# Kernel tuning notes

Measured on AMD Instinct MI355X. Metric: run time of the kernel, lower is better.

## Reference

```python
import jax, jax.numpy as jnp
import numpy as np

B, S, D = 8, 2048, 256
C, H = 32, 4
HD = D // H  # head_dim = 64


def setup_inputs() -> dict:
    key = jax.random.key(0)
    ks = jax.random.split(key, 12)
    scale = 0.02
    x = jax.random.normal(ks[0], (B, S, D), dtype=jnp.float32)
    conditioning = jax.random.uniform(ks[1], (B, S, C), dtype=jnp.float32)
    Wq_w = jax.random.normal(ks[2], (D, D), dtype=jnp.float32) * scale
    Wq_b = jax.random.normal(ks[3], (D,), dtype=jnp.float32) * scale
    Wv_w = jax.random.normal(ks[4], (D, D), dtype=jnp.float32) * scale
    Wv_b = jax.random.normal(ks[5], (D,), dtype=jnp.float32) * scale
    Wk_w = jax.random.normal(ks[6], (C, D, D), dtype=jnp.float32) * scale  # stacked per-class torch Linear weights [out,in]
    Wk_b = jax.random.normal(ks[7], (C, D), dtype=jnp.float32) * scale
    Wo_w = jax.random.normal(ks[8], (D, D), dtype=jnp.float32) * scale
    Wo_b = jax.random.normal(ks[9], (D,), dtype=jnp.float32) * scale
    return {"x": x, "conditioning": conditioning,
            "Wq_w": Wq_w, "Wq_b": Wq_b, "Wv_w": Wv_w, "Wv_b": Wv_b,
            "Wk_w": Wk_w, "Wk_b": Wk_b, "Wo_w": Wo_w, "Wo_b": Wo_b}


def reference(x, conditioning, Wq_w, Wq_b, Wv_w, Wv_b, Wk_w, Wk_b, Wo_w, Wo_b):
    # torch Linear: y = x @ W.T + b, with W of shape [out, in]
    q = (x @ Wq_w.T + Wq_b).reshape(B, S, H, HD).transpose(0, 2, 1, 3)  # (B,H,S,HD)
    v = (x @ Wv_w.T + Wv_b).reshape(B, S, H, HD).transpose(0, 2, 1, 3)
    # per-class keys: (B,C,S,D)
    class_keys = jnp.einsum('bsd,cfd->bcsf', x, Wk_w) + Wk_b[None, :, None, :]
    # data-dependent weighted sum over classes -> effective key (B,S,D)
    k = jnp.einsum('bsc,bcsf->bsf', conditioning, class_keys)
    k = k.reshape(B, S, H, HD).transpose(0, 2, 1, 3)  # (B,H,S,HD)
    # scaled dot-product attention (dropout_p = 0)
    scale = 1.0 / jnp.sqrt(jnp.float32(HD))
    scores = jnp.einsum('bhqd,bhkd->bhqk', q, k) * scale
    attn = jax.nn.softmax(scores, axis=-1)
    out = jnp.einsum('bhqk,bhkd->bhqd', attn, v)
    out = out.transpose(0, 2, 1, 3).reshape(B, S, D)
    return out @ Wo_w.T + Wo_b
```

## Files before the change

kernel.cpp:

```cpp
#include <hip/hip_runtime.h>
#include <hip/hip_bf16.h>

#define BB 8
#define SS 2048
#define DD 256
#define CC 32
#define HH 4
#define HD 64
#define MTOT (BB*SS)

using bf16    = __hip_bfloat16;
using short8  = __attribute__((ext_vector_type(8))) short;
using short4v = __attribute__((ext_vector_type(4))) short;
using floatx4 = __attribute__((ext_vector_type(4))) float;

#if __has_builtin(__builtin_amdgcn_mfma_f32_16x16x16_bf16)
  #define MFMA_PV16(a,b,c) __builtin_amdgcn_mfma_f32_16x16x16_bf16(a,b,c,0,0,0)
  #define HAVE_PV16 1
#elif __has_builtin(__builtin_amdgcn_mfma_f32_16x16x16bf16_1k)
  #define MFMA_PV16(a,b,c) __builtin_amdgcn_mfma_f32_16x16x16bf16_1k(a,b,c,0,0,0)
  #define HAVE_PV16 1
#else
  #define HAVE_PV16 0
#endif

#if __has_builtin(__builtin_amdgcn_global_load_lds)
  #define HAVE_GLL 1
#else
  #define HAVE_GLL 0
#endif

__device__ inline float bf2f(unsigned short u) {
    union { unsigned int i; float f; } v; v.i = ((unsigned int)u) << 16; return v.f;
}
__device__ inline unsigned short f2bfbits(float f) {
    bf16 h = __float2bfloat16(f);
    return __builtin_bit_cast(unsigned short, h);
}

#define N_X    (MTOT*DD)
#define N_COND (MTOT*CC)
#define N_WQW  (DD*DD)
#define N_WQB  (DD)
#define N_WVW  (DD*DD)
#define N_WVB  (DD)
#define N_WKW  (CC*DD*DD)
#define N_WKB  (CC*DD)
#define N_WOW  (DD*DD)
#define N_WOB  (DD)
#define P0 0
#define P1 (P0+N_X)
#define P2 (P1+N_COND)
#define P3 (P2+N_WQW)
#define P4 (P3+N_WQB)
#define P5 (P4+N_WVW)
#define P6 (P5+N_WVB)
#define P7 (P6+N_WKW)
#define P8 (P7+N_WKB)
#define P9 (P8+N_WOW)
#define PTOT (P9+N_WOB)

__global__ void detect_dtype(const void* x, int* flag)
{
    __shared__ int total;
    if (threadIdx.x == 0) total = 0;
    __syncthreads();
    const float* xf = (const float*)x;
    int cnt = 0;
    for (int i = threadIdx.x; i < 4096; i += 256) {
        float v = fabsf(xf[i]);
        if (v == v && v > 1e-4f && v < 1e4f) cnt++;
    }
    atomicAdd(&total, cnt);
    __syncthreads();
    if (threadIdx.x == 0) *flag = (total > 2048) ? 1 : 0;
}

__global__ void convert_all(const void* s0, const void* s1, const void* s2,
                            const void* s3, const void* s4, const void* s5,
                            const void* s6, const void* s7, const void* s8,
                            const void* s9, bf16* dst, const int* flagp)
{
    const bool f32 = (*flagp != 0);
    size_t i = ((size_t)blockIdx.x * 256 + threadIdx.x) * 8;
    const size_t stride = (size_t)gridDim.x * 256 * 8;
    for (; i < (size_t)PTOT; i += stride) {
        const void* src; size_t off;
        if      (i < P1) { src = s0; off = i - P0; }
        else if (i < P2) { src = s1; off = i - P1; }
        else if (i < P3) { src = s2; off = i - P2; }
        else if (i < P4) { src = s3; off = i - P3; }
        else if (i < P5) { src = s4; off = i - P4; }
        else if (i < P6) { src = s5; off = i - P5; }
        else if (i < P7) { src = s6; off = i - P6; }
        else if (i < P8) { src = s7; off = i - P7; }
        else if (i < P9) { src = s8; off = i - P8; }
        else             { src = s9; off = i - P9; }
        if (f32) {
            const float* s = (const float*)src + off;
            float4 a = *(const float4*)(s);
            float4 b = *(const float4*)(s + 4);
            __align__(16) unsigned short t[8];
            t[0] = f2bfbits(a.x); t[1] = f2bfbits(a.y);
            t[2] = f2bfbits(a.z); t[3] = f2bfbits(a.w);
            t[4] = f2bfbits(b.x); t[5] = f2bfbits(b.y);
            t[6] = f2bfbits(b.z); t[7] = f2bfbits(b.w);
            *(uint4*)(dst + i) = *(const uint4*)t;
        } else {
            *(uint4*)(dst + i) = *(const uint4*)((const unsigned short*)src + off);
        }
    }
}

__launch_bounds__(256, 2)
__global__ void gemm_bias(const bf16* __restrict__ X, const bf16* __restrict__ W,
                          const bf16* __restrict__ bias, void* __restrict__ Yv,
                          const int* __restrict__ flagp, int flex_out, int vt_out)
{
    const int LDT = 264;
    __shared__ __align__(16) unsigned short xs[64 * 264];
    __shared__ __align__(16) unsigned short ws[64 * 264];
    const int t  = threadIdx.x;
    const int m0 = blockIdx.y * 64;
    const int n0 = blockIdx.x * 64;

    for (int i = 0; i < 8; ++i) {
        int c = t + i * 256;
        int row = c >> 5, col = (c & 31) * 8;
        *(uint4*)&xs[row * LDT + col] = *(const uint4*)(X + (size_t)(m0 + row) * DD + col);
        *(uint4*)&ws[row * LDT + col] = *(const uint4*)(W + (size_t)(n0 + row) * DD + col);
    }
    __syncthreads();

    const int w = t >> 6, lane = t & 63;
    const int lrow = lane & 15, lk = (lane >> 4) * 8, rgrp = (lane >> 4) * 4;
    floatx4 acc[4] = {};
    const unsigned short* ax = &xs[(w * 16 + lrow) * LDT + lk];
    for (int kt = 0; kt < 8; ++kt) {
        short8 a = *(const short8*)(ax + kt * 32);
        #pragma unroll
        for (int j = 0; j < 4; ++j) {
            short8 b = *(const short8*)&ws[(j * 16 + lrow) * LDT + kt * 32 + lk];
            acc[j] = __builtin_amdgcn_mfma_f32_16x16x32_bf16(a, b, acc[j], 0, 0, 0);
        }
    }

    if (vt_out) {
        __syncthreads();
        unsigned short* ts = xs;
        #pragma unroll
        for (int j = 0; j < 4; ++j) {
            float bv = __bfloat162float(bias[n0 + j * 16 + lrow]);
            #pragma unroll
            for (int r = 0; r < 4; ++r)
                ts[(j * 16 + lrow) * 72 + w * 16 + rgrp + r] = f2bfbits(acc[j][r] + bv);
        }
        __syncthreads();
        const int bq = m0 >> 11, s0v = m0 & 2047, h = n0 >> 6;
        bf16* dstb = (bf16*)Yv + ((size_t)(bq * HH + h) * HD) * SS + s0v;
        for (int i = 0; i < 2; ++i) {
            int idx = t + i * 256, row = idx >> 3, ch = (idx & 7) * 8;
            *(uint4*)(dstb + (size_t)row * SS + ch) = *(const uint4*)&ts[row * 72 + ch];
        }
        return;
    }

    const bool f32o = flex_out && (*flagp != 0);
    #pragma unroll
    for (int j = 0; j < 4; ++j) {
        int col = n0 + j * 16 + lrow;
        float bv = __bfloat162float(bias[col]);
        #pragma unroll
        for (int r = 0; r < 4; ++r) {
            int row = m0 + w * 16 + rgrp + r;
            float val = acc[j][r] + bv;
            if (f32o) ((float*)Yv)[(size_t)row * DD + col] = val;
            else      ((bf16*)Yv)[(size_t)row * DD + col] = __float2bfloat16(val);
        }
    }
}

__device__ inline void stage_ws4(const bf16* __restrict__ Wc,
                                 unsigned short* wsbuf, int w, int lane)
{
    #pragma unroll
    for (int i = 0; i < 8; ++i) {
        int rr = w * 16 + i * 2 + (lane >> 5);
        int cs = (lane & 31) ^ (rr & 7);
        const bf16* src = Wc + (size_t)rr * DD + cs * 8;
        unsigned short* dst = wsbuf + (size_t)(w * 16 + i * 2) * DD;
#if HAVE_GLL
        __builtin_amdgcn_global_load_lds(
            (const __attribute__((address_space(1))) void*)src,
            (__attribute__((address_space(3))) void*)dst, 16, 0, 0);
#else
        uint4 v = *(const uint4*)src;
        *(uint4*)(dst + (size_t)lane * 8) = v;
#endif
    }
}

__launch_bounds__(256, 2)
__global__ void classkey(const bf16* __restrict__ X, const bf16* __restrict__ Cond,
                         const bf16* __restrict__ Wk, const bf16* __restrict__ Wkb,
                         bf16* __restrict__ Kout)
{
    __shared__ __align__(16) unsigned short ws[2][64 * 256];
    __shared__ __align__(16) unsigned short conds[128 * 32];
    __shared__ __align__(16) unsigned short kbs[32 * 64];
    const int t    = threadIdx.x;
    const int w    = t >> 6;
    const int lane = t & 63;
    const int r16  = lane & 15;
    const int quad = lane >> 4;
    const int m0   = blockIdx.y * 128;
    const int n0   = blockIdx.x * 64;

    #pragma unroll
    for (int i = 0; i < 2; ++i) {
        int chunk = t + i * 256;
        int row = chunk >> 2, c8 = (chunk & 3) * 8;
        *(uint4*)&conds[row * 32 + c8] = *(const uint4*)(Cond + (size_t)(m0 + row) * CC + c8);
    }
    {
        int row = t >> 3, c8 = (t & 7) * 8;
        *(uint4*)&kbs[row * 64 + c8] = *(const uint4*)(Wkb + (size_t)row * DD + n0 + c8);
    }

    short8 xa[2][8];
    #pragma unroll
    for (int mt = 0; mt < 2; ++mt) {
        const bf16* xrow = X + (size_t)(m0 + w * 32 + mt * 16 + r16) * DD + quad * 8;
        #pragma unroll
        for (int kt = 0; kt < 8; ++kt)
            xa[mt][kt] = *(const short8*)(xrow + kt * 32);
    }

    stage_ws4(Wk + (size_t)n0 * DD, &ws[0][0], w, lane);

    floatx4 acck[2][4] = {};
    for (int c = 0; c < CC; ++c) {
        __syncthreads();
        if (c + 1 < CC)
            stage_ws4(Wk + (size_t)(c + 1) * DD * DD + (size_t)n0 * DD,
                      &ws[(c + 1) & 1][0], w, lane);

        const unsigned short* wb = &ws[c & 1][0];
        floatx4 p[2][4] = {};
        #pragma unroll
        for (int kt = 0; kt < 8; ++kt) {
            short8 bj[4];
            #pragma unroll
            for (int j = 0; j < 4; ++j)
                bj[j] = *(const short8*)&wb[(j * 16 + r16) * DD +
                                            (((kt * 4 + quad) ^ (r16 & 7)) << 3)];
            #pragma unroll
            for (int mt = 0; mt < 2; ++mt)
                #pragma unroll
                for (int j = 0; j < 4; ++j)
                    p[mt][j] = __builtin_amdgcn_mfma_f32_16x16x32_bf16(xa[mt][kt], bj[j], p[mt][j], 0, 0, 0);
        }
        #pragma unroll
        for (int mt = 0; mt < 2; ++mt)
            #pragma unroll
            for (int r = 0; r < 4; ++r) {
                float cv = bf2f(conds[(w * 32 + mt * 16 + quad * 4 + r) * 32 + c]);
                #pragma unroll
                for (int j = 0; j < 4; ++j) acck[mt][j][r] += cv * p[mt][j][r];
            }
    }

    float kbv[2][4][4] = {};
    for (int c = 0; c < CC; ++c) {
        #pragma unroll
        for (int mt = 0; mt < 2; ++mt)
            #pragma unroll
            for (int r = 0; r < 4; ++r) {
                float cf = bf2f(conds[(w * 32 + mt * 16 + quad * 4 + r) * 32 + c]);
                #pragma unroll
                for (int j = 0; j < 4; ++j)
                    kbv[mt][j][r] += cf * bf2f(kbs[c * 64 + j * 16 + r16]);
            }
    }
    #pragma unroll
    for (int mt = 0; mt < 2; ++mt)
        #pragma unroll
        for (int j = 0; j < 4; ++j) {
            int col = n0 + j * 16 + r16;
            #pragma unroll
            for (int r = 0; r < 4; ++r) {
                int row = m0 + w * 32 + mt * 16 + quad * 4 + r;
                Kout[(size_t)row * DD + col] = __float2bfloat16(acck[mt][j][r] + kbv[mt][j][r]);
            }
        }
}

__device__ inline void stage_kv(const bf16* __restrict__ kRow,
                                const bf16* __restrict__ vRow,
                                unsigned short* kbuf, unsigned short* vbuf,
                                int w, int lane)
{
    int r  = w * 8 + (lane >> 3);
    int cs = (lane & 7) ^ (r & 7);
#if HAVE_GLL
    __builtin_amdgcn_global_load_lds(
        (const __attribute__((address_space(1))) void*)(kRow + (size_t)r * DD + cs * 8),
        (__attribute__((address_space(3))) void*)(kbuf + w * 512), 16, 0, 0);
    __builtin_amdgcn_global_load_lds(
        (const __attribute__((address_space(1))) void*)(vRow + (size_t)r * SS + cs * 8),
        (__attribute__((address_space(3))) void*)(vbuf + w * 512), 16, 0, 0);
#else
    *(uint4*)(kbuf + w * 512 + (size_t)lane * 8) = *(const uint4*)(kRow + (size_t)r * DD + cs * 8);
    *(uint4*)(vbuf + w * 512 + (size_t)lane * 8) = *(const uint4*)(vRow + (size_t)r * SS + cs * 8);
#endif
}

__launch_bounds__(512, 4)
__global__ void attn(const bf16* __restrict__ Q, const bf16* __restrict__ Kb,
                     const bf16* __restrict__ VT, bf16* __restrict__ O)
{
    __shared__ __align__(16) unsigned short ks[2][64 * 64];
    __shared__ __align__(16) unsigned short vt[2][64 * 64];
#if !HAVE_PV16
    __shared__ __align__(16) unsigned short ps[128 * 72];
#endif
    const int t    = threadIdx.x;
    const int w    = t >> 6;
    const int lane = t & 63;
    const int r16  = lane & 15;
    const int quad = lane >> 4;
    const int bh   = blockIdx.y;
    const int b    = bh >> 2, h = bh & 3;
    const int q0   = blockIdx.x * 128;
    const size_t base  = ((size_t)b * SS) * DD + h * HD;
    const size_t vbase = (size_t)bh * HD * SS;

    short8 qa[2];
    {
        const bf16* qrow = Q + base + (size_t)(q0 + w * 16 + r16) * DD + quad * 8;
        #pragma unroll
        for (int k2 = 0; k2 < 2; ++k2) {
            short8 raw = *(const short8*)(qrow + k2 * 32);
            short8 sc;
            #pragma unroll
            for (int e = 0; e < 8; ++e)
                sc[e] = (short)f2bfbits(bf2f((unsigned short)raw[e]) * 0.125f);
            qa[k2] = sc;
        }
    }

    stage_kv(Kb + base, VT + vbase, &ks[0][0], &vt[0][0], w, lane);

    floatx4 acco[4] = {};
    float mrun = -1e30f, lrun = 0.f;

    for (int kt = 0; kt < SS / 64; ++kt) {
        __syncthreads();
        if (kt + 1 < SS / 64)
            stage_kv(Kb + base + (size_t)(kt + 1) * 64 * DD,
                     VT + vbase + (size_t)(kt + 1) * 64,
                     &ks[(kt + 1) & 1][0], &vt[(kt + 1) & 1][0], w, lane);

        const unsigned short* kbuf = &ks[kt & 1][0];
        const unsigned short* vbuf = &vt[kt & 1][0];

        floatx4 s[4] = {};
        #pragma unroll
        for (int k2 = 0; k2 < 2; ++k2) {
            short8 bq = qa[k2];
            #pragma unroll
            for (int j = 0; j < 4; ++j) {
                short8 ak = *(const short8*)&kbuf[(j * 16 + r16) * 64 +
                                                  (((k2 * 4 + quad) ^ (r16 & 7)) << 3)];
                s[j] = __builtin_amdgcn_mfma_f32_16x16x32_bf16(ak, bq, s[j], 0, 0, 0);
            }
        }

        float mx = -1e30f;
        #pragma unroll
        for (int j = 0; j < 4; ++j)
            #pragma unroll
            for (int r = 0; r < 4; ++r) mx = fmaxf(mx, s[j][r]);
        mx = fmaxf(mx, __shfl_xor(mx, 16, 64));
        mx = fmaxf(mx, __shfl_xor(mx, 32, 64));
        float mnew  = fmaxf(mrun, mx);
        float alpha = __expf(mrun - mnew);
        float sum = 0.f;
        #pragma unroll
        for (int j = 0; j < 4; ++j)
            #pragma unroll
            for (int r = 0; r < 4; ++r) {
                float e = __expf(s[j][r] - mnew);
                s[j][r] = e; sum += e;
            }
        sum += __shfl_xor(sum, 16, 64);
        sum += __shfl_xor(sum, 32, 64);
        lrun = lrun * alpha + sum;
        mrun = mnew;

        #pragma unroll
        for (int r = 0; r < 4; ++r) {
            float ar = __shfl(alpha, (quad << 4) + quad * 4 + r, 64);
            #pragma unroll
            for (int jn = 0; jn < 4; ++jn) acco[jn][r] *= ar;
        }

#if HAVE_PV16
        #pragma unroll
        for (int j = 0; j < 4; ++j) {
            short4v p;
            p[0] = (short)f2bfbits(s[j][0]); p[1] = (short)f2bfbits(s[j][1]);
            p[2] = (short)f2bfbits(s[j][2]); p[3] = (short)f2bfbits(s[j][3]);
            #pragma unroll
            for (int jn = 0; jn < 4; ++jn) {
                short4v vv = *(const short4v*)&vbuf[(jn * 16 + r16) * 64 +
                                                    ((((j * 2) + (quad >> 1)) ^ (r16 & 7)) << 3) +
                                                    (quad & 1) * 4];
                acco[jn] = MFMA_PV16(p, vv, acco[jn]);
            }
        }
#else
        #pragma unroll
        for (int j = 0; j < 4; ++j)
            #pragma unroll
            for (int r = 0; r < 4; ++r)
                ps[(w * 16 + r16) * 72 + j * 16 + quad * 4 + r] = f2bfbits(s[j][r]);
        #pragma unroll
        for (int k2 = 0; k2 < 2; ++k2) {
            short8 a = *(const short8*)&ps[(w * 16 + r16) * 72 + k2 * 32 + quad * 8];
            #pragma unroll
            for (int jn = 0; jn < 4; ++jn) {
                short8 bb = *(const short8*)&vbuf[(jn * 16 + r16) * 64 +
                                                  (((k2 * 4 + quad) ^ (r16 & 7)) << 3)];
                acco[jn] = __builtin_amdgcn_mfma_f32_16x16x32_bf16(a, bb, acco[jn], 0, 0, 0);
            }
        }
#endif
    }

    #pragma unroll
    for (int r = 0; r < 4; ++r) {
        float lr = __shfl(lrun, (quad << 4) + quad * 4 + r, 64);
        float inv = 1.0f / lr;
        int row = q0 + w * 16 + quad * 4 + r;
        #pragma unroll
        for (int jn = 0; jn < 4; ++jn)
            O[base + (size_t)row * DD + jn * 16 + r16] = __float2bfloat16(acco[jn][r] * inv);
    }
}

extern "C" void kernel_launch(void* const* d_in, const int* in_sizes, int n_in,
                              void* d_out, int out_size, void* d_ws, size_t ws_size,
                              hipStream_t stream)
{
    int*  flag = (int*)d_ws;
    bf16* conv = (bf16*)((char*)d_ws + 256);

    const bf16* xb    = conv + P0;
    const bf16* condb = conv + P1;
    const bf16* wqw   = conv + P2;
    const bf16* wqb   = conv + P3;
    const bf16* wvw   = conv + P4;
    const bf16* wvb   = conv + P5;
    const bf16* wkw   = conv + P6;
    const bf16* wkb   = conv + P7;
    const bf16* wow   = conv + P8;
    const bf16* wob   = conv + P9;

    bf16* qb = conv + PTOT;
    bf16* kb = qb + (size_t)MTOT * DD;
    bf16* vb = kb + (size_t)MTOT * DD;
    bf16* ob = vb + (size_t)MTOT * DD;

    dim3 blk(256);
    hipLaunchKernelGGL(detect_dtype, dim3(1), blk, 0, stream, d_in[0], flag);
    hipLaunchKernelGGL(convert_all, dim3((PTOT / 8 + 255) / 256), blk, 0, stream,
                       d_in[0], d_in[1], d_in[2], d_in[3], d_in[4],
                       d_in[5], d_in[6], d_in[7], d_in[8], d_in[9],
                       conv, flag);

    dim3 gg(DD / 64, MTOT / 64);
    hipLaunchKernelGGL(gemm_bias, gg, blk, 0, stream, xb, wqw, wqb, (void*)qb, flag, 0, 0);
    hipLaunchKernelGGL(gemm_bias, gg, blk, 0, stream, xb, wvw, wvb, (void*)vb, flag, 0, 1);
    dim3 gck(DD / 64, MTOT / 128);
    hipLaunchKernelGGL(classkey, gck, dim3(256), 0, stream, xb, condb, wkw, wkb, kb);
    dim3 ga(SS / 128, BB * HH);
    hipLaunchKernelGGL(attn, ga, dim3(512), 0, stream, qb, kb, vb, ob);
    hipLaunchKernelGGL(gemm_bias, gg, blk, 0, stream, ob, wow, wob, d_out, flag, 1, 0);
}
```

Before: 260.0 us.

## Fuse Q, V projections and class-key kernel into one heterogeneous launch

Merges the Q GEMM, V GEMM and class-key kernels into a single launch of 2560 blocks. Blocks are interleaved so that every fifth block computes a class-key tile and the other four compute Q or V GEMM tiles, sharing one shared-memory buffer. The aim is to remove two launch gaps and overlap the heavy class-key work with the lighter GEMM tiles. In exchange, every block reserves the larger class-key shared-memory footprint, which may reduce occupancy for the GEMM tiles.

```diff
diff --git a/kernel.cpp b/kernel.cpp
--- a/kernel.cpp
+++ b/kernel.cpp
@@ -112,17 +112,15 @@
     }
 }
 
-__launch_bounds__(256, 2)
-__global__ void gemm_bias(const bf16* __restrict__ X, const bf16* __restrict__ W,
-                          const bf16* __restrict__ bias, void* __restrict__ Yv,
-                          const int* __restrict__ flagp, int flex_out, int vt_out)
+__device__ __forceinline__ void gemm_body(const bf16* __restrict__ X, const bf16* __restrict__ W,
+                                          const bf16* __restrict__ bias, void* __restrict__ Yv,
+                                          const int* __restrict__ flagp, int flex_out, int vt_out,
+                                          unsigned short* smem, int m0, int n0)
 {
     const int LDT = 264;
-    __shared__ __align__(16) unsigned short xs[64 * 264];
-    __shared__ __align__(16) unsigned short ws[64 * 264];
-    const int t  = threadIdx.x;
-    const int m0 = blockIdx.y * 64;
-    const int n0 = blockIdx.x * 64;
+    unsigned short* xs = smem;
+    unsigned short* ws = smem + 64 * 264;
+    const int t = threadIdx.x;
 
     for (int i = 0; i < 8; ++i) {
         int c = t + i * 256;
@@ -180,8 +178,8 @@
     }
 }
 
-__device__ inline void stage_ws4(const bf16* __restrict__ Wc,
-                                 unsigned short* wsbuf, int w, int lane)
+__device__ __forceinline__ void stage_ws4(const bf16* __restrict__ Wc,
+                                          unsigned short* wsbuf, int w, int lane)
 {
     #pragma unroll
     for (int i = 0; i < 8; ++i) {
@@ -200,21 +198,20 @@
     }
 }
 
-__launch_bounds__(256, 2)
-__global__ void classkey(const bf16* __restrict__ X, const bf16* __restrict__ Cond,
-                         const bf16* __restrict__ Wk, const bf16* __restrict__ Wkb,
-                         bf16* __restrict__ Kout)
-{
-    __shared__ __align__(16) unsigned short ws[2][64 * 256];
-    __shared__ __align__(16) unsigned short conds[128 * 32];
-    __shared__ __align__(16) unsigned short kbs[32 * 64];
+__device__ __forceinline__ void classkey_body(const bf16* __restrict__ X, const bf16* __restrict__ Cond,
+                                              const bf16* __restrict__ Wk, const bf16* __restrict__ Wkb,
+                                              bf16* __restrict__ Kout,
+                                              unsigned short* smem, int m0, int n0)
+{
+    unsigned short* ws0   = smem;
+    unsigned short* ws1   = smem + 64 * 256;
+    unsigned short* conds = smem + 2 * 64 * 256;
+    unsigned short* kbs   = conds + 128 * 32;
     const int t    = threadIdx.x;
     const int w    = t >> 6;
     const int lane = t & 63;
     const int r16  = lane & 15;
     const int quad = lane >> 4;
-    const int m0   = blockIdx.y * 128;
-    const int n0   = blockIdx.x * 64;
 
     #pragma unroll
     for (int i = 0; i < 2; ++i) {
@@ -236,16 +233,16 @@
             xa[mt][kt] = *(const short8*)(xrow + kt * 32);
     }
 
-    stage_ws4(Wk + (size_t)n0 * DD, &ws[0][0], w, lane);
+    stage_ws4(Wk + (size_t)n0 * DD, ws0, w, lane);
 
     floatx4 acck[2][4] = {};
     for (int c = 0; c < CC; ++c) {
         __syncthreads();
         if (c + 1 < CC)
             stage_ws4(Wk + (size_t)(c + 1) * DD * DD + (size_t)n0 * DD,
-                      &ws[(c + 1) & 1][0], w, lane);
-
-        const unsigned short* wb = &ws[c & 1][0];
+                      ((c + 1) & 1) ? ws1 : ws0, w, lane);
+
+        const unsigned short* wb = (c & 1) ? ws1 : ws0;
         floatx4 p[2][4] = {};
         #pragma unroll
         for (int kt = 0; kt < 8; ++kt) {
@@ -293,6 +290,42 @@
                 Kout[(size_t)row * DD + col] = __float2bfloat16(acck[mt][j][r] + kbv[mt][j][r]);
             }
         }
+}
+
+__launch_bounds__(256, 2)
+__global__ void fused_qvk(const bf16* __restrict__ X, const bf16* __restrict__ Cond,
+                          const bf16* __restrict__ Wk, const bf16* __restrict__ Wkb,
+                          bf16* __restrict__ Kout,
+                          const bf16* __restrict__ Wqw, const bf16* __restrict__ Wqb, bf16* __restrict__ Qout,
+                          const bf16* __restrict__ Wvw, const bf16* __restrict__ Wvb, bf16* __restrict__ Vout,
+                          const int* __restrict__ flagp)
+{
+    __shared__ __align__(16) unsigned short smem[2 * 64 * 256 + 128 * 32 + 32 * 64];
+    const int bid = blockIdx.x;
+    const int grp = bid / 5, rem = bid % 5;
+    if (rem == 0) {
+        int n0 = (grp & 3) * 64, m0 = (grp >> 2) * 128;
+        classkey_body(X, Cond, Wk, Wkb, Kout, smem, m0, n0);
+    } else {
+        int gi = grp * 4 + (rem - 1);
+        if (gi < 1024) {
+            int n0 = (gi & 3) * 64, m0 = (gi >> 2) * 64;
+            gemm_body(X, Wqw, Wqb, (void*)Qout, flagp, 0, 0, smem, m0, n0);
+        } else {
+            gi -= 1024;
+            int n0 = (gi & 3) * 64, m0 = (gi >> 2) * 64;
+            gemm_body(X, Wvw, Wvb, (void*)Vout, flagp, 0, 1, smem, m0, n0);
+        }
+    }
+}
+
+__launch_bounds__(256, 2)
+__global__ void gemm_bias(const bf16* __restrict__ X, const bf16* __restrict__ W,
+                          const bf16* __restrict__ bias, void* __restrict__ Yv,
+                          const int* __restrict__ flagp, int flex_out, int vt_out)
+{
+    __shared__ __align__(16) unsigned short smem[2 * 64 * 264];
+    gemm_body(X, W, bias, Yv, flagp, flex_out, vt_out, smem, blockIdx.y * 64, blockIdx.x * 64);
 }
 
 __device__ inline void stage_kv(const bf16* __restrict__ kRow,
@@ -479,12 +512,13 @@
                        d_in[5], d_in[6], d_in[7], d_in[8], d_in[9],
                        conv, flag);
 
-    dim3 gg(DD / 64, MTOT / 64);
-    hipLaunchKernelGGL(gemm_bias, gg, blk, 0, stream, xb, wqw, wqb, (void*)qb, flag, 0, 0);
-    hipLaunchKernelGGL(gemm_bias, gg, blk, 0, stream, xb, wvw, wvb, (void*)vb, flag, 0, 1);
-    dim3 gck(DD / 64, MTOT / 128);
-    hipLaunchKernelGGL(classkey, gck, dim3(256), 0, stream, xb, condb, wkw, wkb, kb);
+    hipLaunchKernelGGL(fused_qvk, dim3(2560), blk, 0, stream,
+                       xb, condb, wkw, wkb, kb,
+                       wqw, wqb, qb, wvw, wvb, vb, flag);
+
     dim3 ga(SS / 128, BB * HH);
     hipLaunchKernelGGL(attn, ga, dim3(512), 0, stream, qb, kb, vb, ob);
+
+    dim3 gg(DD / 64, MTOT / 64);
     hipLaunchKernelGGL(gemm_bias, gg, blk, 0, stream, ob, wow, wob, d_out, flag, 1, 0);
 }
```

Measured after the change: 273.9 us. 5.4% more time.
